# Kernel tuning notes

Hardware: AMD Instinct MI355X
Metric: run time of the kernel (lower is better)

## Reference

```python
import jax, jax.numpy as jnp
import numpy as np

RADIUS = 0.08       # float radius -> patches_radius float branch
K = 32              # patch_size_source; spacing = 0 so topk k == K


def setup_inputs() -> dict:
    key = jax.random.key(0)
    k1, k2, k3, k4 = jax.random.split(key, 4)
    B, Ns, Nt = 2, 2048, 32768  # Nt = 32**3 (perfect cube for H_t reshape)
    return {
        "source": jax.random.normal(k1, (B, Ns, 3), dtype=jnp.float32),
        "target": jax.random.normal(k2, (B, Nt, 3), dtype=jnp.float32),
        "source_density": jax.random.uniform(k3, (B, Ns, 1), dtype=jnp.float32),
        "target_density": jax.random.uniform(k4, (B, Nt, 1), dtype=jnp.float32),
    }


def reference(source, target, source_density, target_density):
    B, Ns, _ = source.shape
    Nt = target.shape[1]

    # pairwise squared distances: (B, Nt, Ns)
    r0 = jnp.sum(target * target, axis=2, keepdims=True)            # B,Nt,1
    r1 = jnp.sum(source * source, axis=2, keepdims=True)            # B,Ns,1
    sq_dist = r0 - 2.0 * jnp.einsum('btc,bsc->bts', target, source) + jnp.swapaxes(r1, 1, 2)

    # computed in the original forward but never used downstream (dead value)
    _sq_dist_sel = sq_dist / (jnp.einsum('bti,bsi->bts', target_density, source_density) + 1e-8)

    # top-k nearest neighbors (spacing == 0)
    neg_vals, idx = jax.lax.top_k(-sq_dist, K)                      # B,Nt,K
    sq_pd = -neg_vals

    rad = RADIUS * jnp.ones((B, 1, 1), dtype=sq_dist.dtype)
    valid = (rad ** 2) >= sq_pd                                     # B,Nt,K (rad broadcast)
    idx = jnp.where(valid, idx, -1)

    b_idx = jnp.arange(B)[:, None, None]                            # B,1,1
    src_s = source / (rad + 1e-6)
    tgt_s = target / (rad + 1e-6)

    safe = jnp.maximum(idx, 0)
    patches = jnp.where(valid[..., None], src_s[b_idx, safe], 0.0)  # B,Nt,K,3
    patches = patches - tgt_s[:, :, None, :]
    density = jnp.where(valid[..., None], source_density[b_idx, safe], 0.0)  # B,Nt,K,1

    # gather of an all-ones (B,Ns) mask == validity indicator
    patch_valid = valid.astype(patches.dtype)
    patches_size = jnp.sum(patch_valid, axis=-1)                    # B,Nt

    patches_dist = jnp.sqrt(jnp.maximum(sq_pd, 1e-9)) / (rad + 1e-6)  # B,Nt,K

    mask_cnt = jnp.sum((idx < 0).astype(jnp.int32), axis=-1, keepdims=True)  # B,Nt,1
    weight_density = jnp.sum(density, axis=-2) / mask_cnt            # B,Nt,1

    H = int(round(Nt ** (1.0 / 3.0)))
    patches_idx = jnp.stack([jnp.broadcast_to(b_idx, (B, Nt, K)), idx], axis=-1)

    return (
        patches.reshape(B, H, H, H, K, 3),        # patches source
        patches_idx.reshape(B, H, H, H, K, 2),    # patches idx source
        patches_size,                              # patches size source
        rad,                                       # patches radius source
        patches_dist.reshape(B, H, H, H, K),       # patches dist source
        weight_density,                            # weighted density
    )
```

## Files before the change

### kernel.cpp

```cpp
#include <hip/hip_runtime.h>
#include <math.h>

constexpr int B_  = 2;
constexpr int NS_ = 2048;
constexpr int NT_ = 32768;
constexpr int K_  = 32;
#define RADIUS_F 0.08f

constexpr int TPB = 512;
constexpr int TGT_PER_WAVE = 8;
constexpr int TGT_PER_BLOCK = 8 * TGT_PER_WAVE;
constexpr int BLOCKS_PER_BATCH = NT_ / TGT_PER_BLOCK;
constexpr int NCHUNK = NS_ / 64;

constexpr long long SZ_PATCH = (long long)B_ * NT_ * K_ * 3;
constexpr long long SZ_IDX   = (long long)B_ * NT_ * K_ * 2;
constexpr long long SZ_SIZE  = (long long)B_ * NT_;
constexpr long long SZ_RAD   = B_;
constexpr long long SZ_DIST  = (long long)B_ * NT_ * K_;
constexpr long long O_PATCH = 0;
constexpr long long O_IDX   = O_PATCH + SZ_PATCH;
constexpr long long O_SIZE  = O_IDX + SZ_IDX;
constexpr long long O_RAD   = O_SIZE + SZ_SIZE;
constexpr long long O_DIST  = O_RAD + SZ_RAD;
constexpr long long O_WD    = O_DIST + SZ_DIST;

constexpr unsigned long long tm_mask(int k, int j) {
    unsigned long long m = 0;
    for (int l = 0; l < 64; ++l)
        if (((l & k) == 0) == ((l & j) == 0)) m |= 1ull << l;
    return m;
}

__device__ __forceinline__ float readlane_f(float v, int l) {
    return __int_as_float(__builtin_amdgcn_readlane(__float_as_int(v), l));
}
__device__ __forceinline__ float bperm_f(int addr, float v) {
    return __int_as_float(__builtin_amdgcn_ds_bpermute(addr, __float_as_int(v)));
}
__device__ __forceinline__ float shr1_f(float v) {
    return __int_as_float(__builtin_amdgcn_update_dpp(0, __float_as_int(v),
                                                      0x138, 0xF, 0xF, true));
}
__device__ __forceinline__ float med3_vsv(float pv, int vbits, float lv) {
    float r;
    asm("v_med3_f32 %0, %1, %2, %3" : "=v"(r) : "v"(pv), "s"(vbits), "v"(lv));
    return r;
}
__device__ __forceinline__ float maxs_f(float p, int wbits) {
    float r;
    asm("v_max_f32 %0, %1, %2" : "=v"(r) : "s"(wbits), "v"(p));
    return r;
}
__device__ __forceinline__ float min3_f(float a, float b, float c) {
    float r;
    asm("v_min3_f32 %0, %1, %2, %3" : "=v"(r) : "v"(a), "v"(b), "v"(c));
    return r;
}
__device__ __forceinline__ void cnds(float& lv, float pv, unsigned long long keep) {
    float r;
    asm("v_cndmask_b32 %0, %2, %1, %3" : "=v"(r) : "v"(lv), "v"(pv), "s"(keep));
    lv = r;
}
__device__ __forceinline__ float dist_f(float tx, float ty, float tz, float r0, float4 sp) {
    float dot = __fadd_rn(__fadd_rn(__fmul_rn(tx, sp.x), __fmul_rn(ty, sp.y)), __fmul_rn(tz, sp.z));
    return __fadd_rn(__fsub_rn(r0, __fmul_rn(2.0f, dot)), sp.w);
}

#define BSTG(LV, AJ, K, J) { \
    constexpr unsigned long long tm_ = tm_mask(K, J); \
    float pv_ = bperm_f(AJ, LV); \
    unsigned long long sm_ = __ballot((LV) < pv_); \
    cnds(LV, pv_, ~(sm_ ^ tm_)); \
}
#define S8(AJ, K, J) { BSTG(sa0, AJ, K, J) BSTG(sa1, AJ, K, J) BSTG(sa2, AJ, K, J) BSTG(sa3, AJ, K, J) \
                       BSTG(sb0, AJ, K, J) BSTG(sb1, AJ, K, J) BSTG(sb2, AJ, K, J) BSTG(sb3, AJ, K, J) }
#define C4(AJ, J) { BSTG(sa0, AJ, 128, J) BSTG(sa1, AJ, 128, J) BSTG(sa2, AJ, 128, J) BSTG(sa3, AJ, 128, J) }

#define REC(D, RV, RI, NV, BASE) { \
    unsigned long long mr_ = __ballot(r2f >= (D)); \
    while (mr_) { \
        int sl_ = (int)__builtin_ctzll(mr_); mr_ &= mr_ - 1; \
        float v_ = readlane_f(D, sl_); \
        if (lane == (NV)) { RV = v_; RI = (BASE) + sl_; } \
        ++(NV); \
    } \
}

#define INS2(D, LV, T) { \
    unsigned long long m_ = __ballot((D) < (T)); \
    while (m_) { \
        const int sl1_ = (int)__builtin_ctzll(m_); m_ &= m_ - 1; \
        const int b1_ = __builtin_amdgcn_readlane(__float_as_int(D), sl1_); \
        if (m_) { \
            const int sl2_ = (int)__builtin_ctzll(m_); m_ &= m_ - 1; \
            const int b2_ = __builtin_amdgcn_readlane(__float_as_int(D), sl2_); \
            const int w1_ = (b1_ < b2_) ? b1_ : b2_; \
            const int w2_ = (b1_ < b2_) ? b2_ : b1_; \
            float p1_ = shr1_f(LV); \
            float p2_ = shr1_f(p1_); \
            float t1_ = maxs_f(p1_, w1_); \
            float t2_ = maxs_f(p2_, w2_); \
            LV = min3_f(LV, t1_, t2_); \
        } else { \
            LV = med3_vsv(shr1_f(LV), b1_, LV); \
        } \
    } \
}

__device__ __forceinline__ void epilogue(
    float* __restrict__ out, const float* __restrict__ sden, const float4* ssp,
    int b, long long tb, int lane,
    float lv, float rv, int ri, int nv,
    float tx, float ty, float tz)
{
    const float invdd = 1.0f / (RADIUS_F + 1e-6f);
    int vflag = 0; int vidx = -1; float dsum = 0.f; int vcnt = 0;
    const long long sdb = (long long)b * NS_;
    const int nvc = (nv > 64) ? 64 : nv;
    for (int s = 0; s < nvc; ++s) {
        float vr = readlane_f(rv, s);
        int   ir = __builtin_amdgcn_readlane(ri, s);
        int rank = (int)__popcll(__ballot(lv < vr));
        for (int q = 0; q < s; ++q)
            rank += (readlane_f(rv, q) == vr) ? 1 : 0;
        if (rank < K_) {
            dsum += sden[sdb + ir];
            ++vcnt;
            if (lane == rank) { vflag = 1; vidx = ir; }
        }
    }
    float px = 0.f, py = 0.f, pz = 0.f;
    if (vflag) { float4 spv = ssp[vidx]; px = spv.x; py = spv.y; pz = spv.z; }
    const float tsx = tx * invdd, tsy = ty * invdd, tsz = tz * invdd;
    if (lane < K_) {
        const long long pb = tb * K_ + lane;
        float3 p3;
        p3.x = (vflag ? px * invdd : 0.0f) - tsx;
        p3.y = (vflag ? py * invdd : 0.0f) - tsy;
        p3.z = (vflag ? pz * invdd : 0.0f) - tsz;
        *reinterpret_cast<float3*>(&out[O_PATCH + pb * 3]) = p3;
        float2 ix;
        ix.x = (float)b;
        ix.y = (float)vidx;
        *reinterpret_cast<float2*>(&out[O_IDX + pb * 2]) = ix;
        out[O_DIST + tb * K_ + lane] = sqrtf(fmaxf(lv, 1e-9f)) * invdd;
    }
    if (lane == 0) {
        out[O_SIZE + tb] = (float)vcnt;
        out[O_WD + tb]   = dsum / (float)(K_ - vcnt);
    }
}

__global__ __launch_bounds__(TPB, 8) void group_points_kernel(
    const float* __restrict__ src,
    const float* __restrict__ tgt,
    const float* __restrict__ sden,
    float* __restrict__ out)
{
    __shared__ float4 s_sp[NS_];

    const int tid  = threadIdx.x;
    const int lane = tid & 63;
    const int wav  = tid >> 6;
    const int b    = blockIdx.x / BLOCKS_PER_BATCH;
    const int tile = blockIdx.x % BLOCKS_PER_BATCH;

    for (int j = tid; j < NS_; j += TPB) {
        const float* p = src + ((long long)b * NS_ + j) * 3;
        float x = p[0], y = p[1], z = p[2];
        float r1 = __fadd_rn(__fadd_rn(__fmul_rn(x, x), __fmul_rn(y, y)), __fmul_rn(z, z));
        s_sp[j] = make_float4(x, y, z, r1);
    }
    if (blockIdx.x == 0 && tid == 0) {
        out[O_RAD + 0] = RADIUS_F;
        out[O_RAD + 1] = RADIUS_F;
    }
    __syncthreads();

    const float r2f = __fmul_rn(RADIUS_F, RADIUS_F);
    const int a1  = (lane ^ 1)  << 2;
    const int a2  = (lane ^ 2)  << 2;
    const int a4  = (lane ^ 4)  << 2;
    const int a8  = (lane ^ 8)  << 2;
    const int a16 = (lane ^ 16) << 2;
    const int a32 = (lane ^ 32) << 2;
    const int arev = (63 - lane) << 2;

    for (int gp = 0; gp < TGT_PER_WAVE / 4; ++gp) {
        const int t0 = tile * TGT_PER_BLOCK + wav * TGT_PER_WAVE + gp * 4;
        const long long tb0 = (long long)b * NT_ + t0;
        const float* tp = tgt + tb0 * 3;
        const float tx0 = tp[0],  ty0 = tp[1],  tz0 = tp[2];
        const float tx1 = tp[3],  ty1 = tp[4],  tz1 = tp[5];
        const float tx2 = tp[6],  ty2 = tp[7],  tz2 = tp[8];
        const float tx3 = tp[9],  ty3 = tp[10], tz3 = tp[11];
        const float r00 = __fadd_rn(__fadd_rn(__fmul_rn(tx0, tx0), __fmul_rn(ty0, ty0)), __fmul_rn(tz0, tz0));
        const float r01 = __fadd_rn(__fadd_rn(__fmul_rn(tx1, tx1), __fmul_rn(ty1, ty1)), __fmul_rn(tz1, tz1));
        const float r02 = __fadd_rn(__fadd_rn(__fmul_rn(tx2, tx2), __fmul_rn(ty2, ty2)), __fmul_rn(tz2, tz2));
        const float r03 = __fadd_rn(__fadd_rn(__fmul_rn(tx3, tx3), __fmul_rn(ty3, ty3)), __fmul_rn(tz3, tz3));

        float rv0 = 0.f, rv1 = 0.f, rv2 = 0.f, rv3 = 0.f;
        int   ri0 = 0,   ri1 = 0,   ri2 = 0,   ri3 = 0;
        int   nv0 = 0,   nv1 = 0,   nv2 = 0,   nv3 = 0;

        float4 sp0 = s_sp[lane];
        float4 sp1 = s_sp[64 + lane];
        float sa0 = dist_f(tx0, ty0, tz0, r00, sp0);
        float sa1 = dist_f(tx1, ty1, tz1, r01, sp0);
        float sa2 = dist_f(tx2, ty2, tz2, r02, sp0);
        float sa3 = dist_f(tx3, ty3, tz3, r03, sp0);
        float sb0 = dist_f(tx0, ty0, tz0, r00, sp1);
        float sb1 = dist_f(tx1, ty1, tz1, r01, sp1);
        float sb2 = dist_f(tx2, ty2, tz2, r02, sp1);
        float sb3 = dist_f(tx3, ty3, tz3, r03, sp1);
        REC(sa0, rv0, ri0, nv0, 0)  REC(sb0, rv0, ri0, nv0, 64)
        REC(sa1, rv1, ri1, nv1, 0)  REC(sb1, rv1, ri1, nv1, 64)
        REC(sa2, rv2, ri2, nv2, 0)  REC(sb2, rv2, ri2, nv2, 64)
        REC(sa3, rv3, ri3, nv3, 0)  REC(sb3, rv3, ri3, nv3, 64)
        S8(a1, 2, 1)
        S8(a2, 4, 2)   S8(a1, 4, 1)
        S8(a4, 8, 4)   S8(a2, 8, 2)   S8(a1, 8, 1)
        S8(a8, 16, 8)  S8(a4, 16, 4)  S8(a2, 16, 2)  S8(a1, 16, 1)
        S8(a16, 32, 16) S8(a8, 32, 8) S8(a4, 32, 4)  S8(a2, 32, 2)  S8(a1, 32, 1)
        S8(a32, 64, 32) S8(a16, 64, 16) S8(a8, 64, 8) S8(a4, 64, 4) S8(a2, 64, 2) S8(a1, 64, 1)
        sa0 = fminf(sa0, bperm_f(arev, sb0));
        sa1 = fminf(sa1, bperm_f(arev, sb1));
        sa2 = fminf(sa2, bperm_f(arev, sb2));
        sa3 = fminf(sa3, bperm_f(arev, sb3));
        C4(a32, 32) C4(a16, 16) C4(a8, 8) C4(a4, 4) C4(a2, 2) C4(a1, 1)
        float T0 = readlane_f(sa0, 31);
        float T1 = readlane_f(sa1, 31);
        float T2 = readlane_f(sa2, 31);
        float T3 = readlane_f(sa3, 31);

        for (int c = 2; c < NCHUNK; ++c) {
            float4 sp = s_sp[(c << 6) + lane];
            float d0 = dist_f(tx0, ty0, tz0, r00, sp);
            float d1 = dist_f(tx1, ty1, tz1, r01, sp);
            float d2 = dist_f(tx2, ty2, tz2, r02, sp);
            float d3 = dist_f(tx3, ty3, tz3, r03, sp);
            const int base = c << 6;
            REC(d0, rv0, ri0, nv0, base)
            REC(d1, rv1, ri1, nv1, base)
            REC(d2, rv2, ri2, nv2, base)
            REC(d3, rv3, ri3, nv3, base)
            INS2(d0, sa0, T0)  T0 = readlane_f(sa0, 31);
            INS2(d1, sa1, T1)  T1 = readlane_f(sa1, 31);
            INS2(d2, sa2, T2)  T2 = readlane_f(sa2, 31);
            INS2(d3, sa3, T3)  T3 = readlane_f(sa3, 31);
        }

        epilogue(out, sden, s_sp, b, tb0,     lane, sa0, rv0, ri0, nv0, tx0, ty0, tz0);
        epilogue(out, sden, s_sp, b, tb0 + 1, lane, sa1, rv1, ri1, nv1, tx1, ty1, tz1);
        epilogue(out, sden, s_sp, b, tb0 + 2, lane, sa2, rv2, ri2, nv2, tx2, ty2, tz2);
        epilogue(out, sden, s_sp, b, tb0 + 3, lane, sa3, rv3, ri3, nv3, tx3, ty3, tz3);
    }
}

extern "C" void kernel_launch(void* const* d_in, const int* in_sizes, int n_in,
                              void* d_out, int out_size, void* d_ws, size_t ws_size,
                              hipStream_t stream) {
    const float* src  = (const float*)d_in[0];
    const float* tgt  = (const float*)d_in[1];
    const float* sden = (const float*)d_in[2];
    float* out = (float*)d_out;

    dim3 grid(B_ * BLOCKS_PER_BATCH);
    group_points_kernel<<<grid, TPB, 0, stream>>>(src, tgt, sden, out);
}
```

Baseline: 209.3 us.

## Replace serial top-k insertion with buffered candidate append and bitonic merge

Instead of inserting each candidate below the threshold one or two at a time via DPP shifts, candidates are compacted into a per-wave 64-entry buffer with ds_permute, then bitonic-sorted and merged into the running sorted list when the buffer fills. Compare-exchange steps now use DPP quad permutes for short distances and min/max plus cndmask instead of ballot-based selection. Radius recording is also skipped for chunks where no lane is within radius. The intent is to cut serialized per-candidate work in the early chunks, where many candidates qualify. The cost is full 64-wide sorts on every flush.

Measured after the change: 222.1 us. +6.1%, slower.

```diff
diff --git a/kernel.cpp b/kernel.cpp
--- a/kernel.cpp
+++ b/kernel.cpp
@@ -32,50 +32,95 @@
     return m;
 }
 
+#define INF_F __int_as_float(0x7f800000)
+
 __device__ __forceinline__ float readlane_f(float v, int l) {
     return __int_as_float(__builtin_amdgcn_readlane(__float_as_int(v), l));
 }
 __device__ __forceinline__ float bperm_f(int addr, float v) {
     return __int_as_float(__builtin_amdgcn_ds_bpermute(addr, __float_as_int(v)));
 }
-__device__ __forceinline__ float shr1_f(float v) {
+template<int CTRL>
+__device__ __forceinline__ float dppq_f(float v) {
     return __int_as_float(__builtin_amdgcn_update_dpp(0, __float_as_int(v),
-                                                      0x138, 0xF, 0xF, true));
-}
-__device__ __forceinline__ float med3_vsv(float pv, int vbits, float lv) {
+                                                      CTRL, 0xF, 0xF, true));
+}
+__device__ __forceinline__ float cndf(float a, float b, unsigned long long mask) {
     float r;
-    asm("v_med3_f32 %0, %1, %2, %3" : "=v"(r) : "v"(pv), "s"(vbits), "v"(lv));
+    asm("v_cndmask_b32 %0, %2, %1, %3" : "=v"(r) : "v"(a), "v"(b), "s"(mask));
     return r;
 }
-__device__ __forceinline__ float maxs_f(float p, int wbits) {
-    float r;
-    asm("v_max_f32 %0, %1, %2" : "=v"(r) : "s"(wbits), "v"(p));
+__device__ __forceinline__ int cndi(int a, int b, unsigned long long mask) {
+    int r;
+    asm("v_cndmask_b32 %0, %2, %1, %3" : "=v"(r) : "v"(a), "v"(b), "s"(mask));
     return r;
 }
-__device__ __forceinline__ float min3_f(float a, float b, float c) {
-    float r;
-    asm("v_min3_f32 %0, %1, %2, %3" : "=v"(r) : "v"(a), "v"(b), "v"(c));
-    return r;
-}
-__device__ __forceinline__ void cnds(float& lv, float pv, unsigned long long keep) {
-    float r;
-    asm("v_cndmask_b32 %0, %2, %1, %3" : "=v"(r) : "v"(lv), "v"(pv), "s"(keep));
-    lv = r;
+__device__ __forceinline__ int mbcnt64(unsigned long long m) {
+    return __builtin_amdgcn_mbcnt_hi((unsigned)(m >> 32),
+           __builtin_amdgcn_mbcnt_lo((unsigned)m, 0));
 }
 __device__ __forceinline__ float dist_f(float tx, float ty, float tz, float r0, float4 sp) {
     float dot = __fadd_rn(__fadd_rn(__fmul_rn(tx, sp.x), __fmul_rn(ty, sp.y)), __fmul_rn(tz, sp.z));
     return __fadd_rn(__fsub_rn(r0, __fmul_rn(2.0f, dot)), sp.w);
 }
 
-#define BSTG(LV, AJ, K, J) { \
-    constexpr unsigned long long tm_ = tm_mask(K, J); \
-    float pv_ = bperm_f(AJ, LV); \
-    unsigned long long sm_ = __ballot((LV) < pv_); \
-    cnds(LV, pv_, ~(sm_ ^ tm_)); \
-}
-#define S8(AJ, K, J) { BSTG(sa0, AJ, K, J) BSTG(sa1, AJ, K, J) BSTG(sa2, AJ, K, J) BSTG(sa3, AJ, K, J) \
-                       BSTG(sb0, AJ, K, J) BSTG(sb1, AJ, K, J) BSTG(sb2, AJ, K, J) BSTG(sb3, AJ, K, J) }
-#define C4(AJ, J) { BSTG(sa0, AJ, 128, J) BSTG(sa1, AJ, 128, J) BSTG(sa2, AJ, 128, J) BSTG(sa3, AJ, 128, J) }
+#define CEXD(LV, CTRL, M) { \
+    float p_ = dppq_f<CTRL>(LV); \
+    float mn_ = fminf(LV, p_); \
+    float mx_ = fmaxf(LV, p_); \
+    LV = cndf(mn_, mx_, M); \
+}
+#define CEXB(LV, AJ, M) { \
+    float p_ = bperm_f(AJ, LV); \
+    float mn_ = fminf(LV, p_); \
+    float mx_ = fmaxf(LV, p_); \
+    LV = cndf(mn_, mx_, M); \
+}
+
+#define SORT64(LV) \
+    CEXD(LV, 0xB1, M_2_1) \
+    CEXD(LV, 0x4E, M_4_2)  CEXD(LV, 0xB1, M_4_1) \
+    CEXB(LV, a4, M_8_4)    CEXD(LV, 0x4E, M_8_2)  CEXD(LV, 0xB1, M_8_1) \
+    CEXB(LV, a8, M_16_8)   CEXB(LV, a4, M_16_4)   CEXD(LV, 0x4E, M_16_2)  CEXD(LV, 0xB1, M_16_1) \
+    CEXB(LV, a16, M_32_16) CEXB(LV, a8, M_32_8)   CEXB(LV, a4, M_32_4)    CEXD(LV, 0x4E, M_32_2) CEXD(LV, 0xB1, M_32_1) \
+    CEXB(LV, a32, M_64_32) CEXB(LV, a16, M_64_16) CEXB(LV, a8, M_64_8)    CEXB(LV, a4, M_64_4)   CEXD(LV, 0x4E, M_64_2) CEXD(LV, 0xB1, M_64_1)
+
+#define CLEAN64(LV) \
+    CEXB(LV, a32, M_64_32) CEXB(LV, a16, M_64_16) CEXB(LV, a8, M_64_8) \
+    CEXB(LV, a4, M_64_4)   CEXD(LV, 0x4E, M_64_2) CEXD(LV, 0xB1, M_64_1)
+
+#define FLUSH(LV, BUF, NBUF, T) { \
+    unsigned long long vm_ = ((NBUF) >= 64) ? ~0ull : ((1ull << (NBUF)) - 1ull); \
+    BUF = cndf(BUF, INF_F, vm_); \
+    SORT64(BUF) \
+    float mp_ = bperm_f(arev, BUF); \
+    LV = fminf(LV, mp_); \
+    CLEAN64(LV) \
+    T = readlane_f(LV, 31); \
+    NBUF = 0; \
+}
+
+#define APPEND(D, LV, BUF, NBUF, T) { \
+    unsigned long long m_ = __ballot((D) < (T)); \
+    if (m_) { \
+        int q_ = (int)__popcll(m_); \
+        if ((NBUF) + q_ > 64) { \
+            FLUSH(LV, BUF, NBUF, T) \
+            m_ &= __ballot((D) < (T)); \
+            q_ = (int)__popcll(m_); \
+        } \
+        if (m_) { \
+            int mb_ = mbcnt64(m_); \
+            int sel_ = cndi(mb_, q_ + lane - mb_, m_); \
+            int pm_ = __builtin_amdgcn_ds_permute(((NBUF) + sel_) << 2, __float_as_int(D)); \
+            int hi_ = (NBUF) + q_; \
+            unsigned long long w1_ = (hi_ >= 64) ? ~0ull : ((1ull << hi_) - 1ull); \
+            unsigned long long wm_ = w1_ & ~((1ull << (NBUF)) - 1ull); \
+            BUF = cndf(__int_as_float(pm_), BUF, wm_); \
+            NBUF = hi_; \
+        } \
+    } \
+}
 
 #define REC(D, RV, RI, NV, BASE) { \
     unsigned long long mr_ = __ballot(r2f >= (D)); \
@@ -84,27 +129,6 @@
         float v_ = readlane_f(D, sl_); \
         if (lane == (NV)) { RV = v_; RI = (BASE) + sl_; } \
         ++(NV); \
-    } \
-}
-
-#define INS2(D, LV, T) { \
-    unsigned long long m_ = __ballot((D) < (T)); \
-    while (m_) { \
-        const int sl1_ = (int)__builtin_ctzll(m_); m_ &= m_ - 1; \
-        const int b1_ = __builtin_amdgcn_readlane(__float_as_int(D), sl1_); \
-        if (m_) { \
-            const int sl2_ = (int)__builtin_ctzll(m_); m_ &= m_ - 1; \
-            const int b2_ = __builtin_amdgcn_readlane(__float_as_int(D), sl2_); \
-            const int w1_ = (b1_ < b2_) ? b1_ : b2_; \
-            const int w2_ = (b1_ < b2_) ? b2_ : b1_; \
-            float p1_ = shr1_f(LV); \
-            float p2_ = shr1_f(p1_); \
-            float t1_ = maxs_f(p1_, w1_); \
-            float t2_ = maxs_f(p2_, w2_); \
-            LV = min3_f(LV, t1_, t2_); \
-        } else { \
-            LV = med3_vsv(shr1_f(LV), b1_, LV); \
-        } \
     } \
 }
 
@@ -179,13 +203,17 @@
     __syncthreads();
 
     const float r2f = __fmul_rn(RADIUS_F, RADIUS_F);
-    const int a1  = (lane ^ 1)  << 2;
-    const int a2  = (lane ^ 2)  << 2;
-    const int a4  = (lane ^ 4)  << 2;
-    const int a8  = (lane ^ 8)  << 2;
-    const int a16 = (lane ^ 16) << 2;
-    const int a32 = (lane ^ 32) << 2;
+    const int a4   = (lane ^ 4)  << 2;
+    const int a8   = (lane ^ 8)  << 2;
+    const int a16  = (lane ^ 16) << 2;
+    const int a32  = (lane ^ 32) << 2;
     const int arev = (63 - lane) << 2;
+    const unsigned long long M_2_1   = tm_mask(2, 1);
+    const unsigned long long M_4_2   = tm_mask(4, 2),  M_4_1  = tm_mask(4, 1);
+    const unsigned long long M_8_4   = tm_mask(8, 4),  M_8_2  = tm_mask(8, 2),  M_8_1  = tm_mask(8, 1);
+    const unsigned long long M_16_8  = tm_mask(16, 8), M_16_4 = tm_mask(16, 4), M_16_2 = tm_mask(16, 2), M_16_1 = tm_mask(16, 1);
+    const unsigned long long M_32_16 = tm_mask(32, 16), M_32_8 = tm_mask(32, 8), M_32_4 = tm_mask(32, 4), M_32_2 = tm_mask(32, 2), M_32_1 = tm_mask(32, 1);
+    const unsigned long long M_64_32 = tm_mask(64, 32), M_64_16 = tm_mask(64, 16), M_64_8 = tm_mask(64, 8), M_64_4 = tm_mask(64, 4), M_64_2 = tm_mask(64, 2), M_64_1 = tm_mask(64, 1);
 
     for (int gp = 0; gp < TGT_PER_WAVE / 4; ++gp) {
         const int t0 = tile * TGT_PER_BLOCK + wav * TGT_PER_WAVE + gp * 4;
@@ -200,61 +228,45 @@
         const float r02 = __fadd_rn(__fadd_rn(__fmul_rn(tx2, tx2), __fmul_rn(ty2, ty2)), __fmul_rn(tz2, tz2));
         const float r03 = __fadd_rn(__fadd_rn(__fmul_rn(tx3, tx3), __fmul_rn(ty3, ty3)), __fmul_rn(tz3, tz3));
 
+        float lv0 = INF_F, lv1 = INF_F, lv2 = INF_F, lv3 = INF_F;
+        float bf0 = 0.f, bf1 = 0.f, bf2 = 0.f, bf3 = 0.f;
+        int   nb0 = 0, nb1 = 0, nb2 = 0, nb3 = 0;
+        float T0 = INF_F, T1 = INF_F, T2 = INF_F, T3 = INF_F;
         float rv0 = 0.f, rv1 = 0.f, rv2 = 0.f, rv3 = 0.f;
         int   ri0 = 0,   ri1 = 0,   ri2 = 0,   ri3 = 0;
         int   nv0 = 0,   nv1 = 0,   nv2 = 0,   nv3 = 0;
 
-        float4 sp0 = s_sp[lane];
-        float4 sp1 = s_sp[64 + lane];
-        float sa0 = dist_f(tx0, ty0, tz0, r00, sp0);
-        float sa1 = dist_f(tx1, ty1, tz1, r01, sp0);
-        float sa2 = dist_f(tx2, ty2, tz2, r02, sp0);
-        float sa3 = dist_f(tx3, ty3, tz3, r03, sp0);
-        float sb0 = dist_f(tx0, ty0, tz0, r00, sp1);
-        float sb1 = dist_f(tx1, ty1, tz1, r01, sp1);
-        float sb2 = dist_f(tx2, ty2, tz2, r02, sp1);
-        float sb3 = dist_f(tx3, ty3, tz3, r03, sp1);
-        REC(sa0, rv0, ri0, nv0, 0)  REC(sb0, rv0, ri0, nv0, 64)
-        REC(sa1, rv1, ri1, nv1, 0)  REC(sb1, rv1, ri1, nv1, 64)
-        REC(sa2, rv2, ri2, nv2, 0)  REC(sb2, rv2, ri2, nv2, 64)
-        REC(sa3, rv3, ri3, nv3, 0)  REC(sb3, rv3, ri3, nv3, 64)
-        S8(a1, 2, 1)
-        S8(a2, 4, 2)   S8(a1, 4, 1)
-        S8(a4, 8, 4)   S8(a2, 8, 2)   S8(a1, 8, 1)
-        S8(a8, 16, 8)  S8(a4, 16, 4)  S8(a2, 16, 2)  S8(a1, 16, 1)
-        S8(a16, 32, 16) S8(a8, 32, 8) S8(a4, 32, 4)  S8(a2, 32, 2)  S8(a1, 32, 1)
-        S8(a32, 64, 32) S8(a16, 64, 16) S8(a8, 64, 8) S8(a4, 64, 4) S8(a2, 64, 2) S8(a1, 64, 1)
-        sa0 = fminf(sa0, bperm_f(arev, sb0));
-        sa1 = fminf(sa1, bperm_f(arev, sb1));
-        sa2 = fminf(sa2, bperm_f(arev, sb2));
-        sa3 = fminf(sa3, bperm_f(arev, sb3));
-        C4(a32, 32) C4(a16, 16) C4(a8, 8) C4(a4, 4) C4(a2, 2) C4(a1, 1)
-        float T0 = readlane_f(sa0, 31);
-        float T1 = readlane_f(sa1, 31);
-        float T2 = readlane_f(sa2, 31);
-        float T3 = readlane_f(sa3, 31);
-
-        for (int c = 2; c < NCHUNK; ++c) {
+        for (int c = 0; c < NCHUNK; ++c) {
             float4 sp = s_sp[(c << 6) + lane];
             float d0 = dist_f(tx0, ty0, tz0, r00, sp);
             float d1 = dist_f(tx1, ty1, tz1, r01, sp);
             float d2 = dist_f(tx2, ty2, tz2, r02, sp);
             float d3 = dist_f(tx3, ty3, tz3, r03, sp);
-            const int base = c << 6;
-            REC(d0, rv0, ri0, nv0, base)
-            REC(d1, rv1, ri1, nv1, base)
-            REC(d2, rv2, ri2, nv2, base)
-            REC(d3, rv3, ri3, nv3, base)
-            INS2(d0, sa0, T0)  T0 = readlane_f(sa0, 31);
-            INS2(d1, sa1, T1)  T1 = readlane_f(sa1, 31);
-            INS2(d2, sa2, T2)  T2 = readlane_f(sa2, 31);
-            INS2(d3, sa3, T3)  T3 = readlane_f(sa3, 31);
+
+            float g_ = fminf(fminf(d0, d1), fminf(d2, d3));
+            if (__ballot(g_ <= r2f)) {
+                const int base = c << 6;
+                REC(d0, rv0, ri0, nv0, base)
+                REC(d1, rv1, ri1, nv1, base)
+                REC(d2, rv2, ri2, nv2, base)
+                REC(d3, rv3, ri3, nv3, base)
+            }
+
+            APPEND(d0, lv0, bf0, nb0, T0)
+            APPEND(d1, lv1, bf1, nb1, T1)
+            APPEND(d2, lv2, bf2, nb2, T2)
+            APPEND(d3, lv3, bf3, nb3, T3)
         }
 
-        epilogue(out, sden, s_sp, b, tb0,     lane, sa0, rv0, ri0, nv0, tx0, ty0, tz0);
-        epilogue(out, sden, s_sp, b, tb0 + 1, lane, sa1, rv1, ri1, nv1, tx1, ty1, tz1);
-        epilogue(out, sden, s_sp, b, tb0 + 2, lane, sa2, rv2, ri2, nv2, tx2, ty2, tz2);
-        epilogue(out, sden, s_sp, b, tb0 + 3, lane, sa3, rv3, ri3, nv3, tx3, ty3, tz3);
+        if (nb0) { FLUSH(lv0, bf0, nb0, T0) }
+        if (nb1) { FLUSH(lv1, bf1, nb1, T1) }
+        if (nb2) { FLUSH(lv2, bf2, nb2, T2) }
+        if (nb3) { FLUSH(lv3, bf3, nb3, T3) }
+
+        epilogue(out, sden, s_sp, b, tb0,     lane, lv0, rv0, ri0, nv0, tx0, ty0, tz0);
+        epilogue(out, sden, s_sp, b, tb0 + 1, lane, lv1, rv1, ri1, nv1, tx1, ty1, tz1);
+        epilogue(out, sden, s_sp, b, tb0 + 2, lane, lv2, rv2, ri2, nv2, tx2, ty2, tz2);
+        epilogue(out, sden, s_sp, b, tb0 + 3, lane, lv3, rv3, ri3, nv3, tx3, ty3, tz3);
     }
 }
 
```
